# Kernel optimization log

Measured on AMD Instinct MI355X. Metric: run time of the kernel, lower is better.

## Reference

```python
import jax, jax.numpy as jnp
import numpy as np

B, S, E = 4, 4096, 1024
H = 16
D = E // H  # head_dim = 64


def setup_inputs() -> dict:
    key = jax.random.key(0)
    kx, kk, kq, kv = jax.random.split(key, 4)
    scale = 1.0 / np.sqrt(E)
    return {
        "x": jax.random.normal(kx, (B, S, E), dtype=jnp.float32),
        # torch nn.Linear weight shape: [out_features, in_features] = [D, E]
        "Wk": jax.random.uniform(kk, (D, E), dtype=jnp.float32, minval=-scale, maxval=scale),
        "Wq": jax.random.uniform(kq, (D, E), dtype=jnp.float32, minval=-scale, maxval=scale),
        "Wv": jax.random.uniform(kv, (D, E), dtype=jnp.float32, minval=-scale, maxval=scale),
    }


def reference(x, Wk, Wq, Wv):
    # Projections: x @ W^T  -> [B, S, D]
    k = jnp.einsum('bse,de->bsd', x, Wk)
    q = jnp.einsum('bse,de->bsd', x, Wq)
    v = jnp.einsum('bse,de->bsd', x, Wv)
    # Scaled scores [B, S, S]
    scores = jnp.einsum('bqd,bkd->bqk', q, k) * (D ** -0.5)
    # Causal mask: position q attends to k <= q
    causal = jnp.tril(jnp.ones((S, S), dtype=bool))
    scores = jnp.where(causal, scores, -jnp.inf)
    attn = jax.nn.softmax(scores, axis=-1)
    # dropout omitted (eval mode / attn_pdrop=0)
    out = jnp.einsum('bqk,bkd->bqd', attn, v)
    return out
```

## Files before the change

### kernel.cpp

```cpp
#include <hip/hip_runtime.h>
#include <hip/hip_bf16.h>
#include <stdint.h>

#define BB 4
#define SS 4096
#define EE 1024
#define DD 64

typedef __attribute__((ext_vector_type(8))) short short8;
typedef __attribute__((ext_vector_type(4))) float f32x4;

__device__ inline uint32_t cvtpk(float lo, float hi) {
    uint32_t r;
    asm("v_cvt_pk_bf16_f32 %0, %1, %2" : "=v"(r) : "v"(lo), "v"(hi));
    return r;
}
__device__ inline float bf2f_lo(uint32_t u) {
    union { uint32_t u; float f; } v; v.u = u << 16; return v.f;
}
__device__ inline float bf2f_hi(uint32_t u) {
    union { uint32_t u; float f; } v; v.u = u & 0xFFFF0000u; return v.f;
}

#define GL16(g, l) __builtin_amdgcn_global_load_lds( \
    (const __attribute__((address_space(1))) void*)(g), \
    (__attribute__((address_space(3))) void*)(l), 16, 0, 0)

__global__ __launch_bounds__(256) void wconv_kernel(
    const float* __restrict__ Wq, const float* __restrict__ Wk,
    const float* __restrict__ Wv, ushort* __restrict__ Wb)
{
    int tid = blockIdx.x * 256 + threadIdx.x;
    int sel = tid >> 13;
    int off = (tid & 8191) * 8;
    const float* src = (sel == 0) ? Wq : ((sel == 1) ? Wk : Wv);
    float4 a = *reinterpret_cast<const float4*>(src + off);
    float4 b = *reinterpret_cast<const float4*>(src + off + 4);
    uint4 o;
    o.x = cvtpk(a.x, a.y); o.y = cvtpk(a.z, a.w);
    o.z = cvtpk(b.x, b.y); o.w = cvtpk(b.z, b.w);
    *reinterpret_cast<uint4*>(Wb + (size_t)sel * 65536 + off) = o;
}

__global__ __launch_bounds__(256) void proj_kernel(
    const float* __restrict__ x, const ushort* __restrict__ Wb,
    ushort* __restrict__ q_ws, ushort* __restrict__ k_ws, ushort* __restrict__ vT_ws)
{
    __shared__ __align__(16) char smem[4 * 16384];
    const int t = threadIdx.x;
    const int wid = t >> 6, lane = t & 63, g = lane >> 4, lr = lane & 15;
    const int m0 = blockIdx.x * 32;
    const int NT = EE / 32;

    f32x4 acc[3][2];
#pragma unroll
    for (int ni = 0; ni < 3; ++ni)
#pragma unroll
        for (int mi = 0; mi < 2; ++mi) acc[ni][mi] = (f32x4)(0.0f);

#define PSTAGE(KT, BUFI) do { \
    char* xb_ = smem + (BUFI) * 16384; \
    char* wb_ = xb_ + 4096; \
    int e0_ = (KT) * 32; \
    { \
        int row = t >> 3, c = t & 7; \
        GL16(&x[(size_t)(m0 + row) * EE + e0_ + ((c ^ (row & 7)) << 2)], xb_ + t * 16); \
    } \
    _Pragma("unroll") \
    for (int i = 0; i < 3; ++i) { \
        int v = i * 256 + t; int row = v >> 2, u = v & 3; \
        GL16(&Wb[(size_t)row * EE + e0_ + ((u ^ (row & 3)) << 3)], wb_ + v * 16); \
    } \
} while (0)

    PSTAGE(0, 0); PSTAGE(1, 1); PSTAGE(2, 2); PSTAGE(3, 3);

    for (int kt = 0; kt < NT; ++kt) {
        asm volatile("s_waitcnt vmcnt(12)" ::: "memory");
        __builtin_amdgcn_s_barrier();
        __builtin_amdgcn_sched_barrier(0);

        const char* xb = smem + (kt & 3) * 16384;
        const char* wb = xb + 4096;

        short8 af[3], bf[2];
#pragma unroll
        for (int ni = 0; ni < 3; ++ni) {
            int row = wid * 48 + ni * 16 + lr;
            af[ni] = *reinterpret_cast<const short8*>(wb + row * 64 + ((g ^ (lr & 3)) << 4));
        }
#pragma unroll
        for (int mi = 0; mi < 2; ++mi) {
            int row = mi * 16 + lr;
            int u0 = (2 * g) ^ (lr & 7);
            f32x4 lo = *reinterpret_cast<const f32x4*>(xb + row * 128 + u0 * 16);
            f32x4 hi = *reinterpret_cast<const f32x4*>(xb + row * 128 + (u0 ^ 1) * 16);
            union { short8 s; uint32_t u[4]; } p;
            p.u[0] = cvtpk(lo[0], lo[1]); p.u[1] = cvtpk(lo[2], lo[3]);
            p.u[2] = cvtpk(hi[0], hi[1]); p.u[3] = cvtpk(hi[2], hi[3]);
            bf[mi] = p.s;
        }
#pragma unroll
        for (int ni = 0; ni < 3; ++ni)
#pragma unroll
            for (int mi = 0; mi < 2; ++mi)
                acc[ni][mi] = __builtin_amdgcn_mfma_f32_16x16x32_bf16(af[ni], bf[mi], acc[ni][mi], 0, 0, 0);

        asm volatile("s_waitcnt lgkmcnt(0)" ::: "memory");
        __builtin_amdgcn_sched_barrier(0);
        __builtin_amdgcn_s_barrier();
        __builtin_amdgcn_sched_barrier(0);

        int nx = (kt + 4 < NT) ? kt + 4 : NT - 1;
        PSTAGE(nx, kt & 3);
    }

#pragma unroll
    for (int ni = 0; ni < 3; ++ni) {
        int n0 = wid * 48 + ni * 16 + 4 * g;
        int sel = n0 >> 6, d0 = n0 & 63;
#pragma unroll
        for (int mi = 0; mi < 2; ++mi) {
            int m = m0 + mi * 16 + lr;
            int b = m >> 12, s = m & (SS - 1);
            uint2 p;
            p.x = cvtpk(acc[ni][mi][0], acc[ni][mi][1]);
            p.y = cvtpk(acc[ni][mi][2], acc[ni][mi][3]);
            if (sel == 0) {
                *reinterpret_cast<uint2*>(q_ws + ((size_t)b * SS + s) * DD + d0) = p;
            } else if (sel == 1) {
                *reinterpret_cast<uint2*>(k_ws + ((size_t)b * SS + s) * DD + d0) = p;
            } else {
                vT_ws[((size_t)b * DD + d0 + 0) * SS + s] = (ushort)(p.x & 0xFFFF);
                vT_ws[((size_t)b * DD + d0 + 1) * SS + s] = (ushort)(p.x >> 16);
                vT_ws[((size_t)b * DD + d0 + 2) * SS + s] = (ushort)(p.y & 0xFFFF);
                vT_ws[((size_t)b * DD + d0 + 3) * SS + s] = (ushort)(p.y >> 16);
            }
        }
    }
}

__global__ __launch_bounds__(512) void attn_kernel(
    const ushort* __restrict__ q_ws, const ushort* __restrict__ k_ws,
    const ushort* __restrict__ vT_ws, uint32_t* __restrict__ pO32,
    float* __restrict__ pml)
{
    __shared__ __align__(16) char kv_lds[2][16384];
    const int t = threadIdx.x;
    const int wid = t >> 6, lane = t & 63, g = lane >> 4, lr = lane & 15;
    const int bid = blockIdx.x;
    const int f = bid & 3;
    const int b = (bid >> 2) & 3;
    const int qblk = 31 - (bid >> 4);
    const int qb_w = qblk * 128 + wid * 16;

    const ushort* qp = q_ws + ((size_t)b * SS + qb_w + lr) * DD;
    short8 qf0 = *reinterpret_cast<const short8*>(qp + g * 8);
    short8 qf1 = *reinterpret_cast<const short8*>(qp + 32 + g * 8);

    float m_r = -1e30f, l_r = 0.0f;
    f32x4 acc[4];
#pragma unroll
    for (int i = 0; i < 4; ++i) acc[i] = (f32x4)(0.0f);

    const float sc = 0.125f * 1.44269504f;
    const int nt = 2 * (qblk + 1);
    const int nfull = (qb_w + 1) >> 6;
    const int cs = (nt + 3) >> 2;
    const int t0 = f * cs;
    const int t1 = min(nt, (f + 1) * cs);
    const ushort* kbase = k_ws + (size_t)b * SS * DD;
    const ushort* vbase = vT_ws + (size_t)b * DD * SS;

    const int s0 = g & 1, hi = g >> 1;
    const int idxA = ((lr + 16 * ((s0 << 1) | hi)) << 2);
    const int idxB = idxA ^ 128;

#define ASTAGE(KT, BUFI) do { \
    char* kb_ = kv_lds[BUFI]; \
    int kv0_ = (KT) * 64; \
    { \
        int row = t >> 3, c = t & 7; \
        GL16(kbase + (size_t)(kv0_ + row) * DD + ((c ^ (row & 7)) << 3), kb_ + t * 16); \
        GL16(vbase + (size_t)row * SS + kv0_ + ((c ^ (row & 7)) << 3), kb_ + 8192 + t * 16); \
    } \
} while (0)

    if (t0 < t1) {
        ASTAGE(t0, 0);
        ASTAGE((t0 + 1 < t1) ? t0 + 1 : t0, 1);

        for (int kt = t0; kt < t1; ++kt) {
            const int cur = (kt - t0) & 1;
            asm volatile("s_waitcnt vmcnt(2)" ::: "memory");
            __builtin_amdgcn_s_barrier();
            __builtin_amdgcn_sched_barrier(0);

            const char* kb = kv_lds[cur];
            const char* vb = kb + 8192;
            const int kv0 = kt * 64;

            f32x4 sfr[4];
            __builtin_amdgcn_s_setprio(1);
#pragma unroll
            for (int nf = 0; nf < 4; ++nf) {
                int row = nf * 16 + lr;
                short8 b0 = *reinterpret_cast<const short8*>(kb + row * 128 + ((g ^ (row & 7)) << 4));
                short8 b1 = *reinterpret_cast<const short8*>(kb + row * 128 + (((4 + g) ^ (row & 7)) << 4));
                f32x4 s_ = (f32x4)(0.0f);
                s_ = __builtin_amdgcn_mfma_f32_16x16x32_bf16(b0, qf0, s_, 0, 0, 0);
                s_ = __builtin_amdgcn_mfma_f32_16x16x32_bf16(b1, qf1, s_, 0, 0, 0);
                sfr[nf] = s_;
            }
            __builtin_amdgcn_s_setprio(0);
#pragma unroll
            for (int nf = 0; nf < 4; ++nf) sfr[nf] *= sc;
            if (kt >= nfull) {
#pragma unroll
                for (int nf = 0; nf < 4; ++nf)
#pragma unroll
                    for (int jr = 0; jr < 4; ++jr)
                        if (kv0 + nf * 16 + 4 * g + jr > qb_w + lr) sfr[nf][jr] = -1e30f;
            }
            float mt = fmaxf(fmaxf(fmaxf(sfr[0][0], sfr[0][1]), fmaxf(sfr[0][2], sfr[0][3])),
                             fmaxf(fmaxf(sfr[1][0], sfr[1][1]), fmaxf(sfr[1][2], sfr[1][3])));
            mt = fmaxf(mt, fmaxf(fmaxf(fmaxf(sfr[2][0], sfr[2][1]), fmaxf(sfr[2][2], sfr[2][3])),
                                 fmaxf(fmaxf(sfr[3][0], sfr[3][1]), fmaxf(sfr[3][2], sfr[3][3]))));
            mt = fmaxf(mt, __shfl_xor(mt, 16));
            mt = fmaxf(mt, __shfl_xor(mt, 32));
            float mn = fmaxf(m_r, mt);
            float sf = exp2f(m_r - mn);
            m_r = mn;
            float ps = 0.0f;
            uint32_t pk[8];
#pragma unroll
            for (int nf = 0; nf < 4; ++nf) {
                float e0_ = exp2f(sfr[nf][0] - mn);
                float e1_ = exp2f(sfr[nf][1] - mn);
                float e2_ = exp2f(sfr[nf][2] - mn);
                float e3_ = exp2f(sfr[nf][3] - mn);
                ps += (e0_ + e1_) + (e2_ + e3_);
                pk[nf * 2 + 0] = cvtpk(e0_, e1_);
                pk[nf * 2 + 1] = cvtpk(e2_, e3_);
            }
            ps += __shfl_xor(ps, 16);
            ps += __shfl_xor(ps, 32);
            l_r = l_r * sf + ps;
#pragma unroll
            for (int df = 0; df < 4; ++df) acc[df] *= sf;

            uint32_t pw[2][4];
#pragma unroll
            for (int c = 0; c < 2; ++c) {
                uint32_t r0 = (uint32_t)__builtin_amdgcn_ds_permute(idxA, (int)(s0 ? pk[c * 4 + 2] : pk[c * 4 + 0]));
                uint32_t r1 = (uint32_t)__builtin_amdgcn_ds_permute(idxA, (int)(s0 ? pk[c * 4 + 3] : pk[c * 4 + 1]));
                uint32_t r2 = (uint32_t)__builtin_amdgcn_ds_permute(idxB, (int)(s0 ? pk[c * 4 + 0] : pk[c * 4 + 2]));
                uint32_t r3 = (uint32_t)__builtin_amdgcn_ds_permute(idxB, (int)(s0 ? pk[c * 4 + 1] : pk[c * 4 + 3]));
                pw[c][0] = hi ? r2 : r0;
                pw[c][1] = hi ? r3 : r1;
                pw[c][2] = hi ? r0 : r2;
                pw[c][3] = hi ? r1 : r3;
            }

            __builtin_amdgcn_s_setprio(1);
#pragma unroll
            for (int c = 0; c < 2; ++c) {
                union { uint32_t u[4]; short8 s; } pb;
                pb.u[0] = pw[c][0]; pb.u[1] = pw[c][1];
                pb.u[2] = pw[c][2]; pb.u[3] = pw[c][3];
#pragma unroll
                for (int df = 0; df < 4; ++df) {
                    int row = df * 16 + lr;
                    short8 vb_ = *reinterpret_cast<const short8*>(vb + row * 128 + (((c * 4 + g) ^ (row & 7)) << 4));
                    acc[df] = __builtin_amdgcn_mfma_f32_16x16x32_bf16(vb_, pb.s, acc[df], 0, 0, 0);
                }
            }
            __builtin_amdgcn_s_setprio(0);

            asm volatile("s_waitcnt lgkmcnt(0)" ::: "memory");
            __builtin_amdgcn_sched_barrier(0);
            __builtin_amdgcn_s_barrier();
            __builtin_amdgcn_sched_barrier(0);

            int nx = (kt + 2 < t1) ? kt + 2 : t1 - 1;
            ASTAGE(nx, cur);
        }
    }

    const int pidx = ((b * 256 + qblk * 8 + wid) * 4 + f);
    uint32_t* po = pO32 + (size_t)pidx * 512;
#pragma unroll
    for (int df = 0; df < 4; ++df) {
        po[(df * 8 + 2 * g + 0) * 16 + lr] = cvtpk(acc[df][0], acc[df][1]);
        po[(df * 8 + 2 * g + 1) * 16 + lr] = cvtpk(acc[df][2], acc[df][3]);
    }
    if (g == 0) {
        pml[(size_t)pidx * 32 + lr] = m_r;
        pml[(size_t)pidx * 32 + 16 + lr] = l_r;
    }
}

__global__ __launch_bounds__(64) void combine_kernel(
    const uint32_t* __restrict__ pO32, const float* __restrict__ pml,
    float* __restrict__ out)
{
    const int t = threadIdx.x;
    const int q = t & 15, dblk = t >> 4;
    const int grp = blockIdx.x;
    const int b = grp >> 8, qt = grp & 255;
    const int qb = qt * 16;

    float mf[4], lf[4];
#pragma unroll
    for (int f = 0; f < 4; ++f) {
        mf[f] = pml[(size_t)(grp * 4 + f) * 32 + q];
        lf[f] = pml[(size_t)(grp * 4 + f) * 32 + 16 + q];
    }
    float m = fmaxf(fmaxf(mf[0], mf[1]), fmaxf(mf[2], mf[3]));
    float w[4], l = 0.0f;
#pragma unroll
    for (int f = 0; f < 4; ++f) { w[f] = exp2f(mf[f] - m); l += w[f] * lf[f]; }

    float o[16];
#pragma unroll
    for (int i = 0; i < 16; ++i) o[i] = 0.0f;
#pragma unroll
    for (int f = 0; f < 4; ++f) {
        if (w[f] == 0.0f) continue;
        const uint32_t* src = pO32 + (size_t)(grp * 4 + f) * 512 + dblk * 128 + q;
#pragma unroll
        for (int r0 = 0; r0 < 8; ++r0) {
            uint32_t u = src[r0 * 16];
            o[2 * r0 + 0] += w[f] * bf2f_lo(u);
            o[2 * r0 + 1] += w[f] * bf2f_hi(u);
        }
    }
    float inv = 1.0f / l;
    float* op = out + ((size_t)b * SS + qb + q) * DD + dblk * 16;
#pragma unroll
    for (int i = 0; i < 4; ++i) {
        float4 st;
        st.x = o[4 * i + 0] * inv; st.y = o[4 * i + 1] * inv;
        st.z = o[4 * i + 2] * inv; st.w = o[4 * i + 3] * inv;
        *reinterpret_cast<float4*>(op + 4 * i) = st;
    }
}

extern "C" void kernel_launch(void* const* d_in, const int* in_sizes, int n_in,
                              void* d_out, int out_size, void* d_ws, size_t ws_size,
                              hipStream_t stream) {
    const float* x  = (const float*)d_in[0];
    const float* Wk = (const float*)d_in[1];
    const float* Wq = (const float*)d_in[2];
    const float* Wv = (const float*)d_in[3];
    ushort* q_ws  = (ushort*)d_ws;
    ushort* k_ws  = q_ws + (size_t)BB * SS * DD;
    ushort* vT_ws = k_ws + (size_t)BB * SS * DD;
    ushort* Wb    = vT_ws + (size_t)BB * SS * DD;
    uint32_t* pO32 = (uint32_t*)(Wb + 192 * 1024);
    float* pml     = (float*)(pO32 + (size_t)4096 * 512);
    float* out = (float*)d_out;

    hipLaunchKernelGGL(wconv_kernel, dim3(96), dim3(256), 0, stream, Wq, Wk, Wv, Wb);
    hipLaunchKernelGGL(proj_kernel, dim3(BB * SS / 32), dim3(256), 0, stream,
                       x, Wb, q_ws, k_ws, vT_ws);
    hipLaunchKernelGGL(attn_kernel, dim3(BB * 32 * 4), dim3(512), 0, stream,
                       q_ws, k_ws, vT_ws, pO32, pml);
    hipLaunchKernelGGL(combine_kernel, dim3(BB * SS / 16), dim3(64), 0, stream,
                       pO32, pml, out);
}
```

Measured before the change: 65.73 us.

## Restructure projection GEMM to register-prefetch with bf16 LDS and larger tiles

```diff
diff --git a/kernel.cpp b/kernel.cpp
--- a/kernel.cpp
+++ b/kernel.cpp
@@ -21,6 +21,8 @@
 __device__ inline float bf2f_hi(uint32_t u) {
     union { uint32_t u; float f; } v; v.u = u & 0xFFFF0000u; return v.f;
 }
+
+#define SWZ16(r, bc) ((bc) ^ (((r) & 7) << 4))
 
 #define GL16(g, l) __builtin_amdgcn_global_load_lds( \
     (const __attribute__((address_space(1))) void*)(g), \
@@ -46,73 +48,75 @@
     const float* __restrict__ x, const ushort* __restrict__ Wb,
     ushort* __restrict__ q_ws, ushort* __restrict__ k_ws, ushort* __restrict__ vT_ws)
 {
-    __shared__ __align__(16) char smem[4 * 16384];
+    __shared__ __align__(16) ushort x_lds[64 * 64];
+    __shared__ __align__(16) ushort w_lds[192 * 64];
     const int t = threadIdx.x;
     const int wid = t >> 6, lane = t & 63, g = lane >> 4, lr = lane & 15;
-    const int m0 = blockIdx.x * 32;
-    const int NT = EE / 32;
-
-    f32x4 acc[3][2];
+    const int m0 = blockIdx.x * 64;
+
+    f32x4 acc[3][4];
 #pragma unroll
     for (int ni = 0; ni < 3; ++ni)
 #pragma unroll
-        for (int mi = 0; mi < 2; ++mi) acc[ni][mi] = (f32x4)(0.0f);
-
-#define PSTAGE(KT, BUFI) do { \
-    char* xb_ = smem + (BUFI) * 16384; \
-    char* wb_ = xb_ + 4096; \
-    int e0_ = (KT) * 32; \
-    { \
-        int row = t >> 3, c = t & 7; \
-        GL16(&x[(size_t)(m0 + row) * EE + e0_ + ((c ^ (row & 7)) << 2)], xb_ + t * 16); \
-    } \
+        for (int mi = 0; mi < 4; ++mi) acc[ni][mi] = (f32x4)(0.0f);
+
+    float4 xr[4];
+    uint4 wr[6];
+
+#define LOADX(E0) do { \
     _Pragma("unroll") \
-    for (int i = 0; i < 3; ++i) { \
-        int v = i * 256 + t; int row = v >> 2, u = v & 3; \
-        GL16(&Wb[(size_t)row * EE + e0_ + ((u ^ (row & 3)) << 3)], wb_ + v * 16); \
+    for (int i = 0; i < 4; ++i) { \
+        int idx = i * 256 + t; int row = idx >> 4, c4 = idx & 15; \
+        xr[i] = *reinterpret_cast<const float4*>(&x[(size_t)(m0 + row) * EE + (E0) + c4 * 4]); \
     } \
 } while (0)
-
-    PSTAGE(0, 0); PSTAGE(1, 1); PSTAGE(2, 2); PSTAGE(3, 3);
-
-    for (int kt = 0; kt < NT; ++kt) {
-        asm volatile("s_waitcnt vmcnt(12)" ::: "memory");
-        __builtin_amdgcn_s_barrier();
-        __builtin_amdgcn_sched_barrier(0);
-
-        const char* xb = smem + (kt & 3) * 16384;
-        const char* wb = xb + 4096;
-
-        short8 af[3], bf[2];
-#pragma unroll
-        for (int ni = 0; ni < 3; ++ni) {
-            int row = wid * 48 + ni * 16 + lr;
-            af[ni] = *reinterpret_cast<const short8*>(wb + row * 64 + ((g ^ (lr & 3)) << 4));
-        }
-#pragma unroll
-        for (int mi = 0; mi < 2; ++mi) {
-            int row = mi * 16 + lr;
-            int u0 = (2 * g) ^ (lr & 7);
-            f32x4 lo = *reinterpret_cast<const f32x4*>(xb + row * 128 + u0 * 16);
-            f32x4 hi = *reinterpret_cast<const f32x4*>(xb + row * 128 + (u0 ^ 1) * 16);
-            union { short8 s; uint32_t u[4]; } p;
-            p.u[0] = cvtpk(lo[0], lo[1]); p.u[1] = cvtpk(lo[2], lo[3]);
-            p.u[2] = cvtpk(hi[0], hi[1]); p.u[3] = cvtpk(hi[2], hi[3]);
-            bf[mi] = p.s;
-        }
+#define LOADW(E0) do { \
+    _Pragma("unroll") \
+    for (int i = 0; i < 6; ++i) { \
+        int idx = i * 256 + t; int row = idx >> 3, c8 = idx & 7; \
+        wr[i] = *reinterpret_cast<const uint4*>(&Wb[(size_t)row * EE + (E0) + c8 * 8]); \
+    } \
+} while (0)
+
+    LOADX(0); LOADW(0);
+    for (int e0 = 0; e0 < EE; e0 += 64) {
+#pragma unroll
+        for (int i = 0; i < 4; ++i) {
+            int idx = i * 256 + t; int row = idx >> 4, c4 = idx & 15;
+            uint2 p; p.x = cvtpk(xr[i].x, xr[i].y); p.y = cvtpk(xr[i].z, xr[i].w);
+            *reinterpret_cast<uint2*>((char*)x_lds + row * 128 + SWZ16(row, c4 * 8)) = p;
+        }
+#pragma unroll
+        for (int i = 0; i < 6; ++i) {
+            int idx = i * 256 + t; int row = idx >> 3, c8 = idx & 7;
+            *reinterpret_cast<uint4*>((char*)w_lds + row * 128 + SWZ16(row, c8 * 16)) = wr[i];
+        }
+        __syncthreads();
+        if (e0 + 64 < EE) { LOADX(e0 + 64); LOADW(e0 + 64); }
+
+        short8 af[3][2], bf[4][2];
 #pragma unroll
         for (int ni = 0; ni < 3; ++ni)
 #pragma unroll
-            for (int mi = 0; mi < 2; ++mi)
-                acc[ni][mi] = __builtin_amdgcn_mfma_f32_16x16x32_bf16(af[ni], bf[mi], acc[ni][mi], 0, 0, 0);
-
-        asm volatile("s_waitcnt lgkmcnt(0)" ::: "memory");
-        __builtin_amdgcn_sched_barrier(0);
-        __builtin_amdgcn_s_barrier();
-        __builtin_amdgcn_sched_barrier(0);
-
-        int nx = (kt + 4 < NT) ? kt + 4 : NT - 1;
-        PSTAGE(nx, kt & 3);
+            for (int c = 0; c < 2; ++c) {
+                int row = wid * 48 + ni * 16 + lr;
+                af[ni][c] = *reinterpret_cast<const short8*>((const char*)w_lds + row * 128 + SWZ16(row, c * 64 + g * 16));
+            }
+#pragma unroll
+        for (int mi = 0; mi < 4; ++mi)
+#pragma unroll
+            for (int c = 0; c < 2; ++c) {
+                int row = mi * 16 + lr;
+                bf[mi][c] = *reinterpret_cast<const short8*>((const char*)x_lds + row * 128 + SWZ16(row, c * 64 + g * 16));
+            }
+#pragma unroll
+        for (int ni = 0; ni < 3; ++ni)
+#pragma unroll
+            for (int mi = 0; mi < 4; ++mi)
+#pragma unroll
+                for (int c = 0; c < 2; ++c)
+                    acc[ni][mi] = __builtin_amdgcn_mfma_f32_16x16x32_bf16(af[ni][c], bf[mi][c], acc[ni][mi], 0, 0, 0);
+        __syncthreads();
     }
 
 #pragma unroll
@@ -120,7 +124,7 @@
         int n0 = wid * 48 + ni * 16 + 4 * g;
         int sel = n0 >> 6, d0 = n0 & 63;
 #pragma unroll
-        for (int mi = 0; mi < 2; ++mi) {
+        for (int mi = 0; mi < 4; ++mi) {
             int m = m0 + mi * 16 + lr;
             int b = m >> 12, s = m & (SS - 1);
             uint2 p;
@@ -362,7 +366,7 @@
     float* out = (float*)d_out;
 
     hipLaunchKernelGGL(wconv_kernel, dim3(96), dim3(256), 0, stream, Wq, Wk, Wv, Wb);
-    hipLaunchKernelGGL(proj_kernel, dim3(BB * SS / 32), dim3(256), 0, stream,
+    hipLaunchKernelGGL(proj_kernel, dim3(BB * SS / 64), dim3(256), 0, stream,
                        x, Wb, q_ws, k_ws, vT_ws);
     hipLaunchKernelGGL(attn_kernel, dim3(BB * 32 * 4), dim3(512), 0, stream,
                        q_ws, k_ws, vT_ws, pO32, pml);
```

New measurement: 80.23 us. 1.22x slower.
